# Performance work log

Measured on AMD Instinct MI355X. Metric: run time of the kernel, lower is better.

The kernel has to match this reference:

```python
import jax, jax.numpy as jnp
import numpy as np

B, N, D, MAX_ATOMS, K = 1024, 50000, 256, 200, 8


def setup_inputs() -> dict:
    key = jax.random.key(0)
    k1, k2, k3, k4 = jax.random.split(key, 4)
    return {
        "query_embedding": jax.random.normal(k1, (B, D), dtype=jnp.float32),
        "memory_embeddings": jax.random.normal(k2, (N, D), dtype=jnp.float32),
        "memory_som_masks": jax.random.uniform(k3, (N, MAX_ATOMS), dtype=jnp.float32),
        "W": jax.random.normal(k4, (D, D), dtype=jnp.float32) / jnp.sqrt(jnp.float32(D)),
        "b": jnp.zeros((D,), dtype=jnp.float32),
        "k": K,
    }


def _to_poincare(x, W, b):
    # Linear + Tanh, then rescale into the Poincare ball (radius <= 0.95)
    h = jnp.tanh(x @ W + b)
    norm = jnp.linalg.norm(h, axis=-1, keepdims=True)
    scale = jnp.where(norm > 0.95, 0.95 / norm, jnp.ones_like(norm))
    return h * scale


def _hyperbolic_distance(x, y):
    # ||x_i - y_j||^2 via expansion (same math as broadcasted diff, no [B,N,D] blowup)
    x_sq = jnp.sum(x * x, axis=-1, keepdims=True)            # [B,1]
    y_sq = jnp.sum(y * y, axis=-1)[None, :]                   # [1,N]
    diff_sq = jnp.maximum(x_sq + y_sq - 2.0 * (x @ y.T), 0.0)  # [B,N]
    denom = (1.0 - x_sq) * (1.0 - y_sq)
    arg = 1.0 + 2.0 * diff_sq / (denom + 1e-8)
    return jnp.arccosh(jnp.maximum(arg, 1.0 + 1e-6))


def reference(query_embedding, memory_embeddings, memory_som_masks, W, b, k):
    query_hyp = _to_poincare(query_embedding, W, b)
    memory_hyp = _to_poincare(memory_embeddings, W, b)
    dists = _hyperbolic_distance(query_hyp, memory_hyp)       # [B,N]
    # smallest-k distances
    neg_top, top_idx = jax.lax.top_k(-dists, k)               # [B,k]
    top_dists = -neg_top
    weights = jax.nn.softmax(-top_dists, axis=-1)             # [B,k]
    som_hints = memory_som_masks[top_idx]                     # [B,k,MAX_ATOMS]
    return weights, som_hints
```

## Files before the change

kernel.cpp:

```cpp
#include <hip/hip_runtime.h>
#include <hip/hip_bf16.h>
#include <math.h>
#include <float.h>

#define B_Q   1024
#define N_M   50000
#define DIM   256
#define ATOMS 200
#define KSEL  8
#define NCHUNK 40
#define CHUNK  1280
#define MT    128
#define NMT   10
#define CPC   8
#define NC    (NCHUNK * CPC)
#define T16   16
#define TROWS 64
#define APX   264

typedef __attribute__((ext_vector_type(8))) short bf16x8;
typedef __attribute__((ext_vector_type(4))) float f32x4;

static __device__ inline unsigned short f2bf(float f) {
  __hip_bfloat16 h = __float2bfloat16(f);
  return *reinterpret_cast<unsigned short*>(&h);
}

static __device__ inline void split3(float x, unsigned short& s1,
                                     unsigned short& s2, unsigned short& s3) {
  __hip_bfloat16 b1 = __float2bfloat16(x);
  float f1 = __bfloat162float(b1);
  float r1 = x - f1;
  __hip_bfloat16 b2 = __float2bfloat16(r1);
  float f2 = __bfloat162float(b2);
  __hip_bfloat16 b3 = __float2bfloat16(r1 - f2);
  s1 = *reinterpret_cast<unsigned short*>(&b1);
  s2 = *reinterpret_cast<unsigned short*>(&b2);
  s3 = *reinterpret_cast<unsigned short*>(&b3);
}

static __device__ inline void split3t(float x, unsigned short& s1,
                                      unsigned short& s2, unsigned short& s3) {
  const unsigned u = __float_as_uint(x);
  s1 = (unsigned short)(u >> 16);
  const float f1 = __uint_as_float(u & 0xffff0000u);
  const float r1 = x - f1;
  const unsigned v = __float_as_uint(r1);
  s2 = (unsigned short)(v >> 16);
  const float f2 = __uint_as_float(v & 0xffff0000u);
  const float r2 = r1 - f2;
  s3 = (unsigned short)(__float_as_uint(r2) >> 16);
}

static __device__ inline float tanh32(float z) {
  float tz = fabsf(z) * 2.885390082f;
  tz = fminf(tz, 120.f);
  const float E = __builtin_amdgcn_exp2f(tz);
  const float T = 1.f - 2.f / (E + 1.f);
  return (z >= 0.f) ? T : -T;
}

__global__ __launch_bounds__(256) void wsplit_kernel(
    const float* __restrict__ W,
    unsigned short* __restrict__ Wt1, unsigned short* __restrict__ Wt2,
    unsigned short* __restrict__ Wt3)
{
  const int n = blockIdx.x;
  const int k = threadIdx.x;
  unsigned short s1, s2, s3;
  split3(W[(size_t)k * DIM + n], s1, s2, s3);
  Wt1[(size_t)n * DIM + k] = s1;
  Wt2[(size_t)n * DIM + k] = s2;
  Wt3[(size_t)n * DIM + k] = s3;
}

__global__ __launch_bounds__(1024) void transform_kernel(
    const float* __restrict__ X, int nrows,
    const unsigned short* __restrict__ Wt1, const unsigned short* __restrict__ Wt2,
    const unsigned short* __restrict__ Wt3, const float* __restrict__ bvec,
    float* __restrict__ H, unsigned short* __restrict__ Hb,
    float2* __restrict__ aux)
{
  __shared__ __align__(16) unsigned short X1s[TROWS * APX];
  __shared__ __align__(16) unsigned short X2s[TROWS * APX];
  __shared__ __align__(16) unsigned short X3s[TROWS * APX];
  __shared__ float red[16][TROWS];
  __shared__ float sArr[TROWS];

  const int t    = threadIdx.x;
  const int lane = t & 63;
  const int wave = t >> 6;
  const int row0 = blockIdx.x * TROWS;

  {
    const int r  = t >> 4;
    const int c0 = (t & 15) * 16;
    int gr = row0 + r; if (gr >= nrows) gr = nrows - 1;
    const float4* src = (const float4*)(X + (size_t)gr * DIM + c0);
    bf16x8 p1[2], p2[2], p3[2];
#pragma unroll
    for (int half = 0; half < 2; ++half) {
#pragma unroll
      for (int v = 0; v < 2; ++v) {
        const float4 x4 = src[half * 2 + v];
        const float xv[4] = {x4.x, x4.y, x4.z, x4.w};
#pragma unroll
        for (int i = 0; i < 4; ++i) {
          unsigned short s1, s2, s3;
          split3t(xv[i], s1, s2, s3);
          p1[half][v * 4 + i] = (short)s1;
          p2[half][v * 4 + i] = (short)s2;
          p3[half][v * 4 + i] = (short)s3;
        }
      }
      *(bf16x8*)(X1s + r * APX + c0 + half * 8) = p1[half];
      *(bf16x8*)(X2s + r * APX + c0 + half * 8) = p2[half];
      *(bf16x8*)(X3s + r * APX + c0 + half * 8) = p3[half];
    }
  }
  __syncthreads();

  const int lx   = lane & 15;
  const int quad = lane >> 4;
  const int n0   = wave * 16;

  f32x4 acc[4];
#pragma unroll
  for (int ms = 0; ms < 4; ++ms) { acc[ms][0] = 0.f; acc[ms][1] = 0.f; acc[ms][2] = 0.f; acc[ms][3] = 0.f; }

  const size_t brow = (size_t)(n0 + lx) * DIM + quad * 8;
  bf16x8 b1c = *(const bf16x8*)(Wt1 + brow);
  bf16x8 b2c = *(const bf16x8*)(Wt2 + brow);
  bf16x8 b3c = *(const bf16x8*)(Wt3 + brow);

#pragma unroll
  for (int ks = 0; ks < 8; ++ks) {
    bf16x8 b1n, b2n, b3n;
    if (ks < 7) {
      const size_t nb = brow + (ks + 1) * 32;
      b1n = *(const bf16x8*)(Wt1 + nb);
      b2n = *(const bf16x8*)(Wt2 + nb);
      b3n = *(const bf16x8*)(Wt3 + nb);
    }
    const int ko = ks * 32 + quad * 8;
#pragma unroll
    for (int ms = 0; ms < 4; ++ms) {
      const int ar = (ms * 16 + lx) * APX + ko;
      const bf16x8 a1 = *(const bf16x8*)(X1s + ar);
      const bf16x8 a2 = *(const bf16x8*)(X2s + ar);
      const bf16x8 a3 = *(const bf16x8*)(X3s + ar);
      acc[ms] = __builtin_amdgcn_mfma_f32_16x16x32_bf16(a1, b1c, acc[ms], 0, 0, 0);
      acc[ms] = __builtin_amdgcn_mfma_f32_16x16x32_bf16(a1, b2c, acc[ms], 0, 0, 0);
      acc[ms] = __builtin_amdgcn_mfma_f32_16x16x32_bf16(a2, b1c, acc[ms], 0, 0, 0);
      acc[ms] = __builtin_amdgcn_mfma_f32_16x16x32_bf16(a1, b3c, acc[ms], 0, 0, 0);
      acc[ms] = __builtin_amdgcn_mfma_f32_16x16x32_bf16(a2, b2c, acc[ms], 0, 0, 0);
      acc[ms] = __builtin_amdgcn_mfma_f32_16x16x32_bf16(a3, b1c, acc[ms], 0, 0, 0);
    }
    b1c = b1n; b2c = b2n; b3c = b3n;
  }

  const float bb = bvec[n0 + lx];
  float h[4][4];
#pragma unroll
  for (int ms = 0; ms < 4; ++ms)
#pragma unroll
    for (int r = 0; r < 4; ++r)
      h[ms][r] = tanh32(acc[ms][r] + bb);

  float p[4][4];
#pragma unroll
  for (int ms = 0; ms < 4; ++ms)
#pragma unroll
    for (int r = 0; r < 4; ++r) p[ms][r] = h[ms][r] * h[ms][r];
#pragma unroll
  for (int off = 1; off < 16; off <<= 1)
#pragma unroll
    for (int ms = 0; ms < 4; ++ms)
#pragma unroll
      for (int r = 0; r < 4; ++r) p[ms][r] += __shfl_xor(p[ms][r], off);
  if (lx == 0)
#pragma unroll
    for (int ms = 0; ms < 4; ++ms)
#pragma unroll
      for (int r = 0; r < 4; ++r) red[wave][ms * 16 + quad * 4 + r] = p[ms][r];
  __syncthreads();

  if (t < TROWS) {
    float nsq = 0.f;
#pragma unroll
    for (int w = 0; w < 16; ++w) nsq += red[w][t];
    const float nrm = sqrtf(nsq);
    sArr[t] = (nrm > 0.95f) ? (0.95f / nrm) : 1.f;
  }
  __syncthreads();

  float u[4][4];
#pragma unroll
  for (int ms = 0; ms < 4; ++ms)
#pragma unroll
    for (int r = 0; r < 4; ++r) {
      const float sc = sArr[ms * 16 + quad * 4 + r];
      u[ms][r] = h[ms][r] * sc;
      p[ms][r] = u[ms][r] * u[ms][r];
    }
#pragma unroll
  for (int off = 1; off < 16; off <<= 1)
#pragma unroll
    for (int ms = 0; ms < 4; ++ms)
#pragma unroll
      for (int r = 0; r < 4; ++r) p[ms][r] += __shfl_xor(p[ms][r], off);
  if (lx == 0)
#pragma unroll
    for (int ms = 0; ms < 4; ++ms)
#pragma unroll
      for (int r = 0; r < 4; ++r) red[wave][ms * 16 + quad * 4 + r] = p[ms][r];

  const int colv = n0 + lx;
  const int ksb  = colv >> 5;
  const int qoff = ((colv >> 3) & 3) * 128 + (colv & 7);
#pragma unroll
  for (int ms = 0; ms < 4; ++ms)
#pragma unroll
    for (int r = 0; r < 4; ++r) {
      const int grow = row0 + ms * 16 + quad * 4 + r;
      if (grow < nrows) {
        H[(size_t)grow * DIM + colv] = u[ms][r];
        Hb[((size_t)((row0 >> 4) + ms) * 8 + ksb) * 512 + qoff + (quad * 4 + r) * 8]
            = f2bf(u[ms][r]);
      }
    }
  __syncthreads();
  if (t < TROWS) {
    const int grow = row0 + t;
    if (grow < nrows) {
      float ysq = 0.f;
#pragma unroll
      for (int w = 0; w < 16; ++w) ysq += red[w][t];
      aux[grow] = make_float2(ysq, 1.f / (1.f - ysq));
    }
  }
}

__global__ __launch_bounds__(256) void score_kernel(
    const unsigned short* __restrict__ Hqb, const unsigned short* __restrict__ Hmb,
    const float2* __restrict__ auxq, const float2* __restrict__ auxm,
    float* __restrict__ cand_s, int* __restrict__ cand_i)
{
  __shared__ __align__(16) unsigned short Afs[16 * 64 * 8];
  __shared__ unsigned long long wtop[4][32][CPC];

  const int t    = threadIdx.x;
  const int lane = t & 63;
  const int wave = t >> 6;
  const int q0   = blockIdx.y * 32;
  const int c    = blockIdx.x;
  const int mbase = c * CHUNK;
  const int lx   = lane & 15;
  const int quad = lane >> 4;

#pragma unroll
  for (int i = 0; i < 4; ++i) {
    const int sl = wave * 4 + i;
    const int ks = sl >> 1, qs = sl & 1;
    const bf16x8 a = *(const bf16x8*)(Hqb + ((size_t)((q0 >> 4) + qs) * 8 + ks) * 512 + (size_t)lane * 8);
    *(bf16x8*)(Afs + ((size_t)sl * 64 + lane) * 8) = a;
  }
  const float xq0 = auxq[q0 +      quad * 4 + 0].x;
  const float xq1 = auxq[q0 +      quad * 4 + 1].x;
  const float xq2 = auxq[q0 +      quad * 4 + 2].x;
  const float xq3 = auxq[q0 +      quad * 4 + 3].x;
  const float xq4 = auxq[q0 + 16 + quad * 4 + 0].x;
  const float xq5 = auxq[q0 + 16 + quad * 4 + 1].x;
  const float xq6 = auxq[q0 + 16 + quad * 4 + 2].x;
  const float xq7 = auxq[q0 + 16 + quad * 4 + 3].x;
  __syncthreads();

  unsigned t0a=0xFFFFFFFFu,t0b=0xFFFFFFFFu,t0c=0xFFFFFFFFu;
  unsigned t1a=0xFFFFFFFFu,t1b=0xFFFFFFFFu,t1c=0xFFFFFFFFu;
  unsigned t2a=0xFFFFFFFFu,t2b=0xFFFFFFFFu,t2c=0xFFFFFFFFu;
  unsigned t3a=0xFFFFFFFFu,t3b=0xFFFFFFFFu,t3c=0xFFFFFFFFu;
  unsigned t4a=0xFFFFFFFFu,t4b=0xFFFFFFFFu,t4c=0xFFFFFFFFu;
  unsigned t5a=0xFFFFFFFFu,t5b=0xFFFFFFFFu,t5c=0xFFFFFFFFu;
  unsigned t6a=0xFFFFFFFFu,t6b=0xFFFFFFFFu,t6c=0xFFFFFFFFu;
  unsigned t7a=0xFFFFFFFFu,t7b=0xFFFFFFFFu,t7c=0xFFFFFFFFu;

  const int colw = wave * 32 + lx;

  const unsigned short* Bp = Hmb + (size_t)((mbase >> 4) + wave * 2) * 4096 + (size_t)lane * 8;
#define LD(OFS) (*(const bf16x8*)(Bp + (OFS)))

#define KSTEP(KS, BA, BB) do {                                                        \
    const bf16x8 a0_ = *(const bf16x8*)(Afs + (((KS) * 2 + 0) * 64 + lane) * 8);      \
    const bf16x8 a1_ = *(const bf16x8*)(Afs + (((KS) * 2 + 1) * 64 + lane) * 8);      \
    acc00 = __builtin_amdgcn_mfma_f32_16x16x32_bf16(a0_, BA, acc00, 0, 0, 0);         \
    acc01 = __builtin_amdgcn_mfma_f32_16x16x32_bf16(a0_, BB, acc01, 0, 0, 0);         \
    acc10 = __builtin_amdgcn_mfma_f32_16x16x32_bf16(a1_, BA, acc10, 0, 0, 0);         \
    acc11 = __builtin_amdgcn_mfma_f32_16x16x32_bf16(a1_, BB, acc11, 0, 0, 0);         \
  } while (0)

#define SCOREU(ACC, R, YM, RO, CODE, XQ, T0, T1, T2) do {                             \
    const float sv_ = fmaxf(fmaf(-2.f, (ACC)[R], (XQ) + (YM)), 0.f) * (RO);           \
    const unsigned k_ = (__float_as_uint(sv_) & 0xFFFFFFE0u) | (unsigned)(CODE);      \
    const unsigned a_ = min(T0, k_);                                                  \
    const unsigned x_ = max(T0, k_);                                                  \
    const unsigned b_ = min(T1, x_);                                                  \
    const unsigned y_ = max(T1, x_);                                                  \
    const unsigned c_ = min(T2, y_);                                                  \
    T0 = a_; T1 = b_; T2 = c_;                                                        \
  } while (0)

#define SCOREM(ACC, R, YM, RO, OK, CODE, XQ, T0, T1, T2) do {                         \
    const float sv_ = fmaxf(fmaf(-2.f, (ACC)[R], (XQ) + (YM)), 0.f) * (RO);           \
    const unsigned kr_ = (__float_as_uint(sv_) & 0xFFFFFFE0u) | (unsigned)(CODE);     \
    const unsigned k_ = (OK) ? kr_ : 0xFFFFFFFFu;                                     \
    const unsigned a_ = min(T0, k_);                                                  \
    const unsigned x_ = max(T0, k_);                                                  \
    const unsigned b_ = min(T1, x_);                                                  \
    const unsigned y_ = max(T1, x_);                                                  \
    const unsigned c_ = min(T2, y_);                                                  \
    T0 = a_; T1 = b_; T2 = c_;                                                        \
  } while (0)

#define SCORE16U(C0, C1) do {                                                         \
    const float ym0 = aux0.x, ro0 = aux0.y;                                           \
    const float ym1 = aux1.x, ro1 = aux1.y;                                           \
    SCOREU(acc00, 0, ym0, ro0, C0, xq0, t0a, t0b, t0c);                               \
    SCOREU(acc00, 1, ym0, ro0, C0, xq1, t1a, t1b, t1c);                               \
    SCOREU(acc00, 2, ym0, ro0, C0, xq2, t2a, t2b, t2c);                               \
    SCOREU(acc00, 3, ym0, ro0, C0, xq3, t3a, t3b, t3c);                               \
    SCOREU(acc01, 0, ym1, ro1, C1, xq0, t0a, t0b, t0c);                               \
    SCOREU(acc01, 1, ym1, ro1, C1, xq1, t1a, t1b, t1c);                               \
    SCOREU(acc01, 2, ym1, ro1, C1, xq2, t2a, t2b, t2c);                               \
    SCOREU(acc01, 3, ym1, ro1, C1, xq3, t3a, t3b, t3c);                               \
    SCOREU(acc10, 0, ym0, ro0, C0, xq4, t4a, t4b, t4c);                               \
    SCOREU(acc10, 1, ym0, ro0, C0, xq5, t5a, t5b, t5c);                               \
    SCOREU(acc10, 2, ym0, ro0, C0, xq6, t6a, t6b, t6c);                               \
    SCOREU(acc10, 3, ym0, ro0, C0, xq7, t7a, t7b, t7c);                               \
    SCOREU(acc11, 0, ym1, ro1, C1, xq4, t4a, t4b, t4c);                               \
    SCOREU(acc11, 1, ym1, ro1, C1, xq5, t5a, t5b, t5c);                               \
    SCOREU(acc11, 2, ym1, ro1, C1, xq6, t6a, t6b, t6c);                               \
    SCOREU(acc11, 3, ym1, ro1, C1, xq7, t7a, t7b, t7c);                               \
  } while (0)

#define SCORE16M(OK0, OK1, C0, C1) do {                                               \
    const float ym0 = aux0.x, ro0 = aux0.y;                                           \
    const float ym1 = aux1.x, ro1 = aux1.y;                                           \
    SCOREM(acc00, 0, ym0, ro0, OK0, C0, xq0, t0a, t0b, t0c);                          \
    SCOREM(acc00, 1, ym0, ro0, OK0, C0, xq1, t1a, t1b, t1c);                          \
    SCOREM(acc00, 2, ym0, ro0, OK0, C0, xq2, t2a, t2b, t2c);                          \
    SCOREM(acc00, 3, ym0, ro0, OK0, C0, xq3, t3a, t3b, t3c);                          \
    SCOREM(acc01, 0, ym1, ro1, OK1, C1, xq0, t0a, t0b, t0c);                          \
    SCOREM(acc01, 1, ym1, ro1, OK1, C1, xq1, t1a, t1b, t1c);                          \
    SCOREM(acc01, 2, ym1, ro1, OK1, C1, xq2, t2a, t2b, t2c);                          \
    SCOREM(acc01, 3, ym1, ro1, OK1, C1, xq3, t3a, t3b, t3c);                          \
    SCOREM(acc10, 0, ym0, ro0, OK0, C0, xq4, t4a, t4b, t4c);                          \
    SCOREM(acc10, 1, ym0, ro0, OK0, C0, xq5, t5a, t5b, t5c);                          \
    SCOREM(acc10, 2, ym0, ro0, OK0, C0, xq6, t6a, t6b, t6c);                          \
    SCOREM(acc10, 3, ym0, ro0, OK0, C0, xq7, t7a, t7b, t7c);                          \
    SCOREM(acc11, 0, ym1, ro1, OK1, C1, xq4, t4a, t4b, t4c);                          \
    SCOREM(acc11, 1, ym1, ro1, OK1, C1, xq5, t5a, t5b, t5c);                          \
    SCOREM(acc11, 2, ym1, ro1, OK1, C1, xq6, t6a, t6b, t6c);                          \
    SCOREM(acc11, 3, ym1, ro1, OK1, C1, xq7, t7a, t7b, t7c);                          \
  } while (0)

  if (c != NCHUNK - 1) {
    int midx = mbase + colw;
    bf16x8 xA0 = LD(0),    xA1 = LD(512),  xA2 = LD(1024), xA3 = LD(1536);
    bf16x8 xB0 = LD(4096), xB1 = LD(4608), xB2 = LD(5120), xB3 = LD(5632);

    for (int mt = 0; mt < NMT - 1; ++mt) {
      bf16x8 yA0 = LD(2048), yA1 = LD(2560), yA2 = LD(3072), yA3 = LD(3584);
      bf16x8 yB0 = LD(6144), yB1 = LD(6656), yB2 = LD(7168), yB3 = LD(7680);
      const float2 aux0 = auxm[midx];
      const float2 aux1 = auxm[midx + 16];

      f32x4 acc00 = {0.f, 0.f, 0.f, 0.f};
      f32x4 acc01 = {0.f, 0.f, 0.f, 0.f};
      f32x4 acc10 = {0.f, 0.f, 0.f, 0.f};
      f32x4 acc11 = {0.f, 0.f, 0.f, 0.f};

      KSTEP(0, xA0, xB0);
      KSTEP(1, xA1, xB1);
      KSTEP(2, xA2, xB2);
      KSTEP(3, xA3, xB3);

      Bp += 8 * 4096;
      xA0 = LD(0);    xA1 = LD(512);  xA2 = LD(1024); xA3 = LD(1536);
      xB0 = LD(4096); xB1 = LD(4608); xB2 = LD(5120); xB3 = LD(5632);

      KSTEP(4, yA0, yB0);
      KSTEP(5, yA1, yB1);
      KSTEP(6, yA2, yB2);
      KSTEP(7, yA3, yB3);

      SCORE16U(mt * 2, mt * 2 + 1);
      midx += MT;
    }

    {
      bf16x8 yA0 = LD(2048), yA1 = LD(2560), yA2 = LD(3072), yA3 = LD(3584);
      bf16x8 yB0 = LD(6144), yB1 = LD(6656), yB2 = LD(7168), yB3 = LD(7680);
      const float2 aux0 = auxm[midx];
      const float2 aux1 = auxm[midx + 16];

      f32x4 acc00 = {0.f, 0.f, 0.f, 0.f};
      f32x4 acc01 = {0.f, 0.f, 0.f, 0.f};
      f32x4 acc10 = {0.f, 0.f, 0.f, 0.f};
      f32x4 acc11 = {0.f, 0.f, 0.f, 0.f};

      KSTEP(0, xA0, xB0);
      KSTEP(1, xA1, xB1);
      KSTEP(2, xA2, xB2);
      KSTEP(3, xA3, xB3);
      KSTEP(4, yA0, yB0);
      KSTEP(5, yA1, yB1);
      KSTEP(6, yA2, yB2);
      KSTEP(7, yA3, yB3);

      SCORE16U((NMT - 1) * 2, (NMT - 1) * 2 + 1);
    }
  } else {
    const int vrem = N_M - mbase;
    const bool ok0 = colw < vrem;
    const bool ok1 = colw + 16 < vrem;
    const int midx = mbase + colw;

    bf16x8 xA0 = LD(0),    xA1 = LD(512),  xA2 = LD(1024), xA3 = LD(1536);
    bf16x8 xB0 = LD(4096), xB1 = LD(4608), xB2 = LD(5120), xB3 = LD(5632);
    bf16x8 yA0 = LD(2048), yA1 = LD(2560), yA2 = LD(3072), yA3 = LD(3584);
    bf16x8 yB0 = LD(6144), yB1 = LD(6656), yB2 = LD(7168), yB3 = LD(7680);
    const float2 aux0 = auxm[midx];
    const float2 aux1 = auxm[midx + 16];

    f32x4 acc00 = {0.f, 0.f, 0.f, 0.f};
    f32x4 acc01 = {0.f, 0.f, 0.f, 0.f};
    f32x4 acc10 = {0.f, 0.f, 0.f, 0.f};
    f32x4 acc11 = {0.f, 0.f, 0.f, 0.f};

    KSTEP(0, xA0, xB0);
    KSTEP(1, xA1, xB1);
    KSTEP(2, xA2, xB2);
    KSTEP(3, xA3, xB3);
    KSTEP(4, yA0, yB0);
    KSTEP(5, yA1, yB1);
    KSTEP(6, yA2, yB2);
    KSTEP(7, yA3, yB3);

    SCORE16M(ok0, ok1, 0, 1);
  }

#undef LD
#undef KSTEP
#undef SCOREU
#undef SCOREM
#undef SCORE16U
#undef SCORE16M

#define K2E(K) ( (((unsigned long long)(K)) << 32) |                                  \
    (unsigned)(mbase + wave * 32 + lx + (((K) & 30u) >> 1) * 128 + ((K) & 1u) * 16) )

#define EXTRACT_ROW(WIDX, T0, T1, T2) do {                                            \
    unsigned long long p0 = K2E(T0), p1 = K2E(T1), p2 = K2E(T2);                      \
    for (int rd = 0; rd < CPC; ++rd) {                                                \
      unsigned long long lm = (p0 < p1) ? p0 : p1;                                    \
      lm = (p2 < lm) ? p2 : lm;                                                       \
      unsigned long long gm = lm;                                                     \
      for (int off = 1; off < 16; off <<= 1) {                                        \
        const unsigned long long o = __shfl_xor(gm, off);                             \
        gm = (o < gm) ? o : gm;                                                       \
      }                                                                               \
      if      (p0 == gm) p0 = ~0ULL;                                                  \
      else if (p1 == gm) p1 = ~0ULL;                                                  \
      else if (p2 == gm) p2 = ~0ULL;                                                  \
      if (lx == 0) wtop[wave][WIDX][rd] = gm;                                         \
    }                                                                                 \
  } while (0)

  EXTRACT_ROW(quad * 4 + 0,      t0a, t0b, t0c);
  EXTRACT_ROW(quad * 4 + 1,      t1a, t1b, t1c);
  EXTRACT_ROW(quad * 4 + 2,      t2a, t2b, t2c);
  EXTRACT_ROW(quad * 4 + 3,      t3a, t3b, t3c);
  EXTRACT_ROW(16 + quad * 4 + 0, t4a, t4b, t4c);
  EXTRACT_ROW(16 + quad * 4 + 1, t5a, t5b, t5c);
  EXTRACT_ROW(16 + quad * 4 + 2, t6a, t6b, t6c);
  EXTRACT_ROW(16 + quad * 4 + 3, t7a, t7b, t7c);
#undef EXTRACT_ROW
#undef K2E
  __syncthreads();

  {
    const int qr = t >> 3;
    const int sp = t & 7;
    unsigned long long v0 = wtop[0][qr][sp];
    unsigned long long v1 = wtop[1][qr][sp];
    unsigned long long v2 = wtop[2][qr][sp];
    unsigned long long v3 = wtop[3][qr][sp];
    const size_t cbase = ((size_t)(q0 + qr) * NCHUNK + c) * CPC;
    for (int rd = 0; rd < CPC; ++rd) {
      unsigned long long lm = (v0 < v1) ? v0 : v1;
      const unsigned long long l2 = (v2 < v3) ? v2 : v3;
      lm = (l2 < lm) ? l2 : lm;
      unsigned long long gm = lm;
#pragma unroll
      for (int off = 1; off < 8; off <<= 1) {
        const unsigned long long o = __shfl_xor(gm, off);
        gm = (o < gm) ? o : gm;
      }
      if      (v0 == gm) v0 = ~0ULL;
      else if (v1 == gm) v1 = ~0ULL;
      else if (v2 == gm) v2 = ~0ULL;
      else if (v3 == gm) v3 = ~0ULL;
      if (sp == 0) {
        cand_s[cbase + rd] = __uint_as_float((unsigned int)(gm >> 32));
        cand_i[cbase + rd] = (int)(unsigned int)(gm & 0xffffffffu);
      }
    }
  }
}

__global__ __launch_bounds__(256) void finalize_kernel(
    const float* __restrict__ Hq, const float* __restrict__ Hm,
    const float* __restrict__ masks,
    const float* __restrict__ cand_s, const int* __restrict__ cand_i,
    float* __restrict__ outW, float* __restrict__ outH)
{
  const int q    = blockIdx.x;
  const int t    = threadIdx.x;
  const int lane = t & 63;
  const int wave = t >> 6;

  __shared__ unsigned long long wtop[4][T16];
  __shared__ int    selIdx[T16];
  __shared__ double dArr[T16];
  __shared__ int    fin_i[KSEL];
  __shared__ double fin_d[KSEL];
  __shared__ double ew[KSEL];

  {
    const size_t base = (size_t)q * NC + (size_t)wave * (NC / 4);
    unsigned long long pk[2];
#pragma unroll
    for (int s = 0; s < 2; ++s) {
      const int c = lane + 64 * s;
      pk[s] = (c < NC / 4)
        ? ((((unsigned long long)__float_as_uint(cand_s[base + c])) << 32) | (unsigned int)cand_i[base + c])
        : ~0ULL;
    }
    for (int r = 0; r < T16; ++r) {
      unsigned long long lm = (pk[0] < pk[1]) ? pk[0] : pk[1];
      unsigned long long gm = lm;
#pragma unroll
      for (int off = 1; off < 64; off <<= 1) {
        unsigned long long o = __shfl_xor(gm, off);
        gm = (o < gm) ? o : gm;
      }
      bool done = false;
#pragma unroll
      for (int s = 0; s < 2; ++s) if (!done && pk[s] == gm) { pk[s] = ~0ULL; done = true; }
      if (lane == 0) wtop[wave][r] = gm;
    }
  }
  __syncthreads();

  if (wave == 0) {
    unsigned long long v = wtop[lane >> 4][lane & 15];
    for (int r = 0; r < T16; ++r) {
      unsigned long long gm = v;
#pragma unroll
      for (int off = 1; off < 64; off <<= 1) {
        unsigned long long o = __shfl_xor(gm, off);
        gm = (o < gm) ? o : gm;
      }
      if (v == gm) v = ~0ULL;
      if (lane == 0) selIdx[r] = (int)(unsigned int)(gm & 0xffffffffULL);
    }
  }
  __syncthreads();

  const float4 q4 = *(const float4*)(Hq + (size_t)q * DIM + 4 * lane);
  double xp_ = (double)q4.x * q4.x + (double)q4.y * q4.y + (double)q4.z * q4.z + (double)q4.w * q4.w;
#pragma unroll
  for (int off = 1; off < 64; off <<= 1) xp_ += __shfl_xor(xp_, off);
  const double xsq = xp_;

  for (int r = wave; r < T16; r += 4) {
    const int cidx = selIdx[r];
    const float4 m4 = *(const float4*)(Hm + (size_t)cidx * DIM + 4 * lane);
    double dp = (double)q4.x * m4.x + (double)q4.y * m4.y + (double)q4.z * m4.z + (double)q4.w * m4.w;
    double yp = (double)m4.x * m4.x + (double)m4.y * m4.y + (double)m4.z * m4.z + (double)m4.w * m4.w;
#pragma unroll
    for (int off = 1; off < 64; off <<= 1) { dp += __shfl_xor(dp, off); yp += __shfl_xor(yp, off); }
    if (lane == 0) {
      double diff = xsq + yp - 2.0 * dp; if (diff < 0.0) diff = 0.0;
      double den = (1.0 - xsq) * (1.0 - yp);
      double arg = 1.0 + 2.0 * diff / (den + 1e-8);
      const double lo = 1.0 + 1e-6;
      if (arg < lo) arg = lo;
      dArr[r] = log(arg + sqrt(arg * arg - 1.0));
    }
  }
  __syncthreads();

  if (t < T16) {
    const double dj = dArr[t]; const int ij = selIdx[t];
    int rank = 0;
#pragma unroll
    for (int i = 0; i < T16; ++i)
      rank += (dArr[i] < dj || (dArr[i] == dj && selIdx[i] < ij)) ? 1 : 0;
    if (rank < KSEL) { fin_d[rank] = dj; fin_i[rank] = ij; }
  }
  __syncthreads();
  if (t < KSEL) ew[t] = exp(fin_d[0] - fin_d[t]);
  __syncthreads();
  if (t < KSEL) {
    double ssum = 0.0;
#pragma unroll
    for (int i = 0; i < KSEL; ++i) ssum += ew[i];
    outW[(size_t)q * KSEL + t] = (float)(ew[t] / ssum);
  }

  const int g  = t >> 5;
  const int l0 = t & 31;
  const int row = fin_i[g];
  for (int l = l0; l < ATOMS; l += 32)
    outH[((size_t)q * KSEL + g) * ATOMS + l] = masks[(size_t)row * ATOMS + l];
}

extern "C" void kernel_launch(void* const* d_in, const int* in_sizes, int n_in,
                              void* d_out, int out_size, void* d_ws, size_t ws_size,
                              hipStream_t stream) {
  const float* Q     = (const float*)d_in[0];
  const float* M     = (const float*)d_in[1];
  const float* masks = (const float*)d_in[2];
  const float* W     = (const float*)d_in[3];
  const float* bv    = (const float*)d_in[4];

  char* w = (char*)d_ws;
  float*          Hq   = (float*)(w);
  float*          Hm   = (float*)(w + 1048576);
  unsigned short* Hqb  = (unsigned short*)(w + 52248576);
  unsigned short* Hmb  = (unsigned short*)(w + 52772864);
  float2*         auxq = (float2*)(w + 78397440);
  float2*         auxm = (float2*)(w + 78405632);
  float*          cs   = (float*)(w + 78806016);
  int*            cix  = (int*)(w + 80116736);

  unsigned short* Wt1 = (unsigned short*)(w + 78806016);
  unsigned short* Wt2 = Wt1 + DIM * DIM;
  unsigned short* Wt3 = Wt2 + DIM * DIM;

  wsplit_kernel<<<DIM, DIM, 0, stream>>>(W, Wt1, Wt2, Wt3);
  transform_kernel<<<(B_Q + TROWS - 1) / TROWS, 1024, 0, stream>>>(Q, B_Q, Wt1, Wt2, Wt3, bv, Hq, Hqb, auxq);
  transform_kernel<<<(N_M + TROWS - 1) / TROWS, 1024, 0, stream>>>(M, N_M, Wt1, Wt2, Wt3, bv, Hm, Hmb, auxm);
  score_kernel<<<dim3(NCHUNK, B_Q / 32), 256, 0, stream>>>(Hqb, Hmb, auxq, auxm, cs, cix);
  finalize_kernel<<<B_Q, 256, 0, stream>>>(Hq, Hm, masks, cs, cix,
                                           (float*)d_out, (float*)d_out + (size_t)B_Q * KSEL);
}
```

Before: 347.1 us.

## Restructure transform kernel so each wave owns a 16-row strip across all columns

The transform kernel now assigns each wave a 16-row strip and computes all 256 output columns in registers, instead of having 16 waves share a 64-row tile staged in LDS. The A operand split is done directly from global memory per k-step, and W is pre-laid out in MFMA fragment order so B loads are coalesced. This removes LDS staging and cross-wave block barriers for the row-norm reduction, which now happens with in-wave shuffles. In exchange each wave re-reads all of the split W from L2/cache and holds 16 accumulators, which raises register pressure.

```diff
diff --git a/kernel.cpp b/kernel.cpp
--- a/kernel.cpp
+++ b/kernel.cpp
@@ -15,8 +15,7 @@
 #define CPC   8
 #define NC    (NCHUNK * CPC)
 #define T16   16
-#define TROWS 64
-#define APX   264
+#define WSTRIP 16
 
 typedef __attribute__((ext_vector_type(8))) short bf16x8;
 typedef __attribute__((ext_vector_type(4))) float f32x4;
@@ -69,174 +68,112 @@
   const int k = threadIdx.x;
   unsigned short s1, s2, s3;
   split3(W[(size_t)k * DIM + n], s1, s2, s3);
-  Wt1[(size_t)n * DIM + k] = s1;
-  Wt2[(size_t)n * DIM + k] = s2;
-  Wt3[(size_t)n * DIM + k] = s3;
-}
-
-__global__ __launch_bounds__(1024) void transform_kernel(
+  const size_t off = ((size_t)(n >> 4) * 8 + (k >> 5)) * 512
+                   + (size_t)(((k >> 3) & 3) * 128 + (n & 15) * 8 + (k & 7));
+  Wt1[off] = s1;
+  Wt2[off] = s2;
+  Wt3[off] = s3;
+}
+
+__global__ __launch_bounds__(256) void transform_kernel(
     const float* __restrict__ X, int nrows,
     const unsigned short* __restrict__ Wt1, const unsigned short* __restrict__ Wt2,
     const unsigned short* __restrict__ Wt3, const float* __restrict__ bvec,
     float* __restrict__ H, unsigned short* __restrict__ Hb,
     float2* __restrict__ aux)
 {
-  __shared__ __align__(16) unsigned short X1s[TROWS * APX];
-  __shared__ __align__(16) unsigned short X2s[TROWS * APX];
-  __shared__ __align__(16) unsigned short X3s[TROWS * APX];
-  __shared__ float red[16][TROWS];
-  __shared__ float sArr[TROWS];
-
   const int t    = threadIdx.x;
   const int lane = t & 63;
   const int wave = t >> 6;
-  const int row0 = blockIdx.x * TROWS;
-
-  {
-    const int r  = t >> 4;
-    const int c0 = (t & 15) * 16;
-    int gr = row0 + r; if (gr >= nrows) gr = nrows - 1;
-    const float4* src = (const float4*)(X + (size_t)gr * DIM + c0);
-    bf16x8 p1[2], p2[2], p3[2];
-#pragma unroll
-    for (int half = 0; half < 2; ++half) {
-#pragma unroll
-      for (int v = 0; v < 2; ++v) {
-        const float4 x4 = src[half * 2 + v];
-        const float xv[4] = {x4.x, x4.y, x4.z, x4.w};
-#pragma unroll
-        for (int i = 0; i < 4; ++i) {
-          unsigned short s1, s2, s3;
-          split3t(xv[i], s1, s2, s3);
-          p1[half][v * 4 + i] = (short)s1;
-          p2[half][v * 4 + i] = (short)s2;
-          p3[half][v * 4 + i] = (short)s3;
-        }
-      }
-      *(bf16x8*)(X1s + r * APX + c0 + half * 8) = p1[half];
-      *(bf16x8*)(X2s + r * APX + c0 + half * 8) = p2[half];
-      *(bf16x8*)(X3s + r * APX + c0 + half * 8) = p3[half];
-    }
-  }
-  __syncthreads();
-
   const int lx   = lane & 15;
   const int quad = lane >> 4;
-  const int n0   = wave * 16;
-
-  f32x4 acc[4];
-#pragma unroll
-  for (int ms = 0; ms < 4; ++ms) { acc[ms][0] = 0.f; acc[ms][1] = 0.f; acc[ms][2] = 0.f; acc[ms][3] = 0.f; }
-
-  const size_t brow = (size_t)(n0 + lx) * DIM + quad * 8;
-  bf16x8 b1c = *(const bf16x8*)(Wt1 + brow);
-  bf16x8 b2c = *(const bf16x8*)(Wt2 + brow);
-  bf16x8 b3c = *(const bf16x8*)(Wt3 + brow);
-
-#pragma unroll
+  const int row0w = (blockIdx.x * 4 + wave) * WSTRIP;
+
+  int gr = row0w + lx; if (gr >= nrows) gr = nrows - 1;
+  const float* Xr = X + (size_t)gr * DIM + quad * 8;
+
+  f32x4 acc[16];
+#pragma unroll
+  for (int nt = 0; nt < 16; ++nt) { acc[nt][0] = 0.f; acc[nt][1] = 0.f;
+                                    acc[nt][2] = 0.f; acc[nt][3] = 0.f; }
+
   for (int ks = 0; ks < 8; ++ks) {
-    bf16x8 b1n, b2n, b3n;
-    if (ks < 7) {
-      const size_t nb = brow + (ks + 1) * 32;
-      b1n = *(const bf16x8*)(Wt1 + nb);
-      b2n = *(const bf16x8*)(Wt2 + nb);
-      b3n = *(const bf16x8*)(Wt3 + nb);
-    }
-    const int ko = ks * 32 + quad * 8;
-#pragma unroll
-    for (int ms = 0; ms < 4; ++ms) {
-      const int ar = (ms * 16 + lx) * APX + ko;
-      const bf16x8 a1 = *(const bf16x8*)(X1s + ar);
-      const bf16x8 a2 = *(const bf16x8*)(X2s + ar);
-      const bf16x8 a3 = *(const bf16x8*)(X3s + ar);
-      acc[ms] = __builtin_amdgcn_mfma_f32_16x16x32_bf16(a1, b1c, acc[ms], 0, 0, 0);
-      acc[ms] = __builtin_amdgcn_mfma_f32_16x16x32_bf16(a1, b2c, acc[ms], 0, 0, 0);
-      acc[ms] = __builtin_amdgcn_mfma_f32_16x16x32_bf16(a2, b1c, acc[ms], 0, 0, 0);
-      acc[ms] = __builtin_amdgcn_mfma_f32_16x16x32_bf16(a1, b3c, acc[ms], 0, 0, 0);
-      acc[ms] = __builtin_amdgcn_mfma_f32_16x16x32_bf16(a2, b2c, acc[ms], 0, 0, 0);
-      acc[ms] = __builtin_amdgcn_mfma_f32_16x16x32_bf16(a3, b1c, acc[ms], 0, 0, 0);
-    }
-    b1c = b1n; b2c = b2n; b3c = b3n;
-  }
-
-  const float bb = bvec[n0 + lx];
-  float h[4][4];
-#pragma unroll
-  for (int ms = 0; ms < 4; ++ms)
+    const float4 xa = *(const float4*)(Xr + ks * 32);
+    const float4 xb = *(const float4*)(Xr + ks * 32 + 4);
+    bf16x8 a1, a2, a3;
+    {
+      const float xv[8] = {xa.x, xa.y, xa.z, xa.w, xb.x, xb.y, xb.z, xb.w};
+#pragma unroll
+      for (int i = 0; i < 8; ++i) {
+        unsigned short s1, s2, s3;
+        split3t(xv[i], s1, s2, s3);
+        a1[i] = (short)s1; a2[i] = (short)s2; a3[i] = (short)s3;
+      }
+    }
+    const size_t bko = (size_t)ks * 512 + (size_t)lane * 8;
+#pragma unroll
+    for (int nt = 0; nt < 16; ++nt) {
+      const size_t bo = (size_t)nt * 4096 + bko;
+      const bf16x8 b1 = *(const bf16x8*)(Wt1 + bo);
+      const bf16x8 b2 = *(const bf16x8*)(Wt2 + bo);
+      const bf16x8 b3 = *(const bf16x8*)(Wt3 + bo);
+      acc[nt] = __builtin_amdgcn_mfma_f32_16x16x32_bf16(a1, b1, acc[nt], 0, 0, 0);
+      acc[nt] = __builtin_amdgcn_mfma_f32_16x16x32_bf16(a1, b2, acc[nt], 0, 0, 0);
+      acc[nt] = __builtin_amdgcn_mfma_f32_16x16x32_bf16(a2, b1, acc[nt], 0, 0, 0);
+      acc[nt] = __builtin_amdgcn_mfma_f32_16x16x32_bf16(a1, b3, acc[nt], 0, 0, 0);
+      acc[nt] = __builtin_amdgcn_mfma_f32_16x16x32_bf16(a2, b2, acc[nt], 0, 0, 0);
+      acc[nt] = __builtin_amdgcn_mfma_f32_16x16x32_bf16(a3, b1, acc[nt], 0, 0, 0);
+    }
+  }
+
+#pragma unroll
+  for (int nt = 0; nt < 16; ++nt) {
+    const float bb = bvec[nt * 16 + lx];
 #pragma unroll
     for (int r = 0; r < 4; ++r)
-      h[ms][r] = tanh32(acc[ms][r] + bb);
-
-  float p[4][4];
-#pragma unroll
-  for (int ms = 0; ms < 4; ++ms)
-#pragma unroll
-    for (int r = 0; r < 4; ++r) p[ms][r] = h[ms][r] * h[ms][r];
+      acc[nt][r] = tanh32(acc[nt][r] + bb);
+  }
+
+  float nsq[4] = {0.f, 0.f, 0.f, 0.f};
+#pragma unroll
+  for (int nt = 0; nt < 16; ++nt)
+#pragma unroll
+    for (int r = 0; r < 4; ++r) nsq[r] += acc[nt][r] * acc[nt][r];
 #pragma unroll
   for (int off = 1; off < 16; off <<= 1)
 #pragma unroll
-    for (int ms = 0; ms < 4; ++ms)
-#pragma unroll
-      for (int r = 0; r < 4; ++r) p[ms][r] += __shfl_xor(p[ms][r], off);
-  if (lx == 0)
-#pragma unroll
-    for (int ms = 0; ms < 4; ++ms)
-#pragma unroll
-      for (int r = 0; r < 4; ++r) red[wave][ms * 16 + quad * 4 + r] = p[ms][r];
-  __syncthreads();
-
-  if (t < TROWS) {
-    float nsq = 0.f;
-#pragma unroll
-    for (int w = 0; w < 16; ++w) nsq += red[w][t];
-    const float nrm = sqrtf(nsq);
-    sArr[t] = (nrm > 0.95f) ? (0.95f / nrm) : 1.f;
-  }
-  __syncthreads();
-
-  float u[4][4];
-#pragma unroll
-  for (int ms = 0; ms < 4; ++ms)
+    for (int r = 0; r < 4; ++r) nsq[r] += __shfl_xor(nsq[r], off);
+
+  float sc[4], ys[4];
+#pragma unroll
+  for (int r = 0; r < 4; ++r) {
+    const float nrm = sqrtf(nsq[r]);
+    sc[r] = (nrm > 0.95f) ? (0.95f / nrm) : 1.f;
+    ys[r] = nsq[r] * sc[r] * sc[r];
+  }
+
+  if (lx == 0) {
 #pragma unroll
     for (int r = 0; r < 4; ++r) {
-      const float sc = sArr[ms * 16 + quad * 4 + r];
-      u[ms][r] = h[ms][r] * sc;
-      p[ms][r] = u[ms][r] * u[ms][r];
-    }
-#pragma unroll
-  for (int off = 1; off < 16; off <<= 1)
-#pragma unroll
-    for (int ms = 0; ms < 4; ++ms)
-#pragma unroll
-      for (int r = 0; r < 4; ++r) p[ms][r] += __shfl_xor(p[ms][r], off);
-  if (lx == 0)
-#pragma unroll
-    for (int ms = 0; ms < 4; ++ms)
-#pragma unroll
-      for (int r = 0; r < 4; ++r) red[wave][ms * 16 + quad * 4 + r] = p[ms][r];
-
-  const int colv = n0 + lx;
-  const int ksb  = colv >> 5;
-  const int qoff = ((colv >> 3) & 3) * 128 + (colv & 7);
-#pragma unroll
-  for (int ms = 0; ms < 4; ++ms)
+      const int grow = row0w + quad * 4 + r;
+      if (grow < nrows) aux[grow] = make_float2(ys[r], 1.f / (1.f - ys[r]));
+    }
+  }
+
+  const int g = row0w >> 4;
+#pragma unroll
+  for (int nt = 0; nt < 16; ++nt) {
+    const int col = nt * 16 + lx;
+    const size_t hbbase = ((size_t)g * 8 + (col >> 5)) * 512
+                        + (size_t)(((col >> 3) & 3) * 128 + (col & 7));
 #pragma unroll
     for (int r = 0; r < 4; ++r) {
-      const int grow = row0 + ms * 16 + quad * 4 + r;
+      const int grow = row0w + quad * 4 + r;
       if (grow < nrows) {
-        H[(size_t)grow * DIM + colv] = u[ms][r];
-        Hb[((size_t)((row0 >> 4) + ms) * 8 + ksb) * 512 + qoff + (quad * 4 + r) * 8]
-            = f2bf(u[ms][r]);
+        const float u = acc[nt][r] * sc[r];
+        H[(size_t)grow * DIM + col] = u;
+        Hb[hbbase + (size_t)(quad * 4 + r) * 8] = f2bf(u);
       }
-    }
-  __syncthreads();
-  if (t < TROWS) {
-    const int grow = row0 + t;
-    if (grow < nrows) {
-      float ysq = 0.f;
-#pragma unroll
-      for (int w = 0; w < 16; ++w) ysq += red[w][t];
-      aux[grow] = make_float2(ysq, 1.f / (1.f - ysq));
     }
   }
 }
@@ -650,8 +587,8 @@
   unsigned short* Wt3 = Wt2 + DIM * DIM;
 
   wsplit_kernel<<<DIM, DIM, 0, stream>>>(W, Wt1, Wt2, Wt3);
-  transform_kernel<<<(B_Q + TROWS - 1) / TROWS, 1024, 0, stream>>>(Q, B_Q, Wt1, Wt2, Wt3, bv, Hq, Hqb, auxq);
-  transform_kernel<<<(N_M + TROWS - 1) / TROWS, 1024, 0, stream>>>(M, N_M, Wt1, Wt2, Wt3, bv, Hm, Hmb, auxm);
+  transform_kernel<<<(B_Q + 4 * WSTRIP - 1) / (4 * WSTRIP), 256, 0, stream>>>(Q, B_Q, Wt1, Wt2, Wt3, bv, Hq, Hqb, auxq);
+  transform_kernel<<<(N_M + 4 * WSTRIP - 1) / (4 * WSTRIP), 256, 0, stream>>>(M, N_M, Wt1, Wt2, Wt3, bv, Hm, Hmb, auxm);
   score_kernel<<<dim3(NCHUNK, B_Q / 32), 256, 0, stream>>>(Hqb, Hmb, auxq, auxm, cs, cix);
   finalize_kernel<<<B_Q, 256, 0, stream>>>(Hq, Hm, masks, cs, cix,
                                            (float*)d_out, (float*)d_out + (size_t)B_Q * KSEL);
```

New measurement: 446.9 us. 1.29x slower.
